# Optimization experiments

Measured on AMD Instinct MI355X. Metric: run time of the kernel, lower is better.

## Reference

```python
import jax, jax.numpy as jnp
import numpy as np

B = 16384
G = 2048   # granule_cell_count
N = 512    # ca3_cell_count
DT = 0.5   # integration_timestep
STEPS = 5  # ca3_attractor_steps
A_REC = 0.02   # recovery_time_constant
B_SUB = 0.2    # subthreshold_coupling
C_RESET = -55.0  # spike_reset_voltage
D_AHP = 4.0      # after_hyperpolarization_jump
CONN_P = 0.1


def setup_inputs() -> dict:
    key = jax.random.key(0)
    k1, k2, k3, k4 = jax.random.split(key, 4)
    dg_query_spikes = (jax.random.uniform(k1, (B, G)) < 0.1).astype(jnp.float32)
    W_mossy = 0.05 * jax.random.normal(k2, (N, G), dtype=jnp.float32)
    mask = (jax.random.uniform(k3, (N, N)) < CONN_P).astype(jnp.float32)
    W_rec = mask * jax.random.uniform(k4, (N, N)) * 0.1
    W_rec = W_rec * (1.0 - jnp.eye(N, dtype=jnp.float32))  # zero diagonal
    v0 = jnp.full((N,), -65.0, dtype=jnp.float32)
    u0 = jnp.full((N,), 0.2 * -65.0, dtype=jnp.float32)
    return {"dg_query_spikes": dg_query_spikes, "W_mossy": W_mossy,
            "W_rec": W_rec, "v0": v0, "u0": u0}


def _izhikevich_step(v, u, I):
    # Euler step of the Izhikevich neuron model, per original torch code.
    dv = 0.04 * v * v + 5.0 * v + 140.0 - u + I
    du = A_REC * (B_SUB * v - u)
    v = v + dv * DT
    u = u + du * DT
    spike = (v >= 30.0).astype(v.dtype)
    v = jnp.where(spike > 0, jnp.asarray(C_RESET, v.dtype), v)
    u = u + spike * D_AHP
    v = jnp.clip(v, -90.0, 30.0)
    return v, u, spike


def reference(dg_query_spikes, W_mossy, W_rec, v0, u0):
    # query_current = Linear(dg) * 10.0  -> [B, N]
    query_current = (dg_query_spikes @ W_mossy.T) * 10.0
    v = jnp.broadcast_to(v0, (B, N))
    u = jnp.broadcast_to(u0, (B, N))
    spike = jnp.zeros((B, N), dtype=jnp.float32)
    for _ in range(STEPS):  # fixed small unrolled recurrence
        # torch.mv(W_rec, spikes) batched: [B,N] @ [N,N]^T
        recurrent_current = (v >= 30.0).astype(jnp.float32) @ W_rec.T
        total_current = query_current + recurrent_current
        v, u, spike = _izhikevich_step(v, u, total_current)
    return spike
```

## Files before the change

### kernel.cpp

```cpp
#include <hip/hip_runtime.h>
#include <cstdint>
#include <cstddef>


typedef __attribute__((ext_vector_type(8))) short bf16x8;
typedef __attribute__((ext_vector_type(8))) unsigned short u16x8;
typedef __attribute__((ext_vector_type(4))) float f32x4;
typedef __attribute__((ext_vector_type(4))) unsigned int u32x4;

constexpr int Bn = 16384, Gn = 2048, Nn = 512;
constexpr int BM = 128, BN = 128, BK = 32;
constexpr int NKT = Gn / BK;
constexpr size_t A_BYTES = (size_t)NKT * 4 * Bn * 16;
constexpr size_t B_BYTES = (size_t)NKT * 3 * 4 * Nn * 16;

__device__ __forceinline__ unsigned short f2bf(float x) {
  uint32_t u = __builtin_bit_cast(uint32_t, x);
  u += 0x7FFFu + ((u >> 16) & 1u);
  return (unsigned short)(u >> 16);
}
__device__ __forceinline__ float bf2f(unsigned short h) {
  return __builtin_bit_cast(float, (uint32_t)h << 16);
}

__device__ __forceinline__ void glds16(const void* g, const void* l) {
  __builtin_amdgcn_global_load_lds(
      (const __attribute__((address_space(1))) unsigned int*)g,
      (__attribute__((address_space(3))) unsigned int*)l, 16, 0, 0);
}

__device__ __forceinline__ float izhi5(float I, float vi, float ui) {
#pragma clang fp contract(off)
  float v = vi, u = ui, spk = 0.0f;
#pragma unroll
  for (int st = 0; st < 5; ++st) {
    float dv = 0.04f * v * v + 5.0f * v + 140.0f - u + I;
    float du = 0.02f * (0.2f * v - u);
    v = v + dv * 0.5f;
    u = u + du * 0.5f;
    spk = (v >= 30.0f) ? 1.0f : 0.0f;
    if (spk > 0.0f) v = -55.0f;
    u = u + spk * 4.0f;
    v = fminf(fmaxf(v, -90.0f), 30.0f);
  }
  return spk;
}

__launch_bounds__(256)
__global__ void prep_dg(const float* __restrict__ dg, unsigned short* __restrict__ Ab) {
  __shared__ uint32_t lds[64][129];
  const int t  = (int)threadIdx.x;
  const int mt = (int)blockIdx.x >> 3;
  const int gt = (int)blockIdx.x & 7;
  const int m0 = mt * 64, g0 = gt * 256;
  {
    const int mm = t >> 2, q = t & 3;
    const float* src = dg + (size_t)(m0 + mm) * Gn + g0;
#pragma unroll
    for (int i = 0; i < 16; ++i) {
      float4 v = *reinterpret_cast<const float4*>(src + i * 16 + q * 4);
      uint32_t a = (v.x != 0.0f ? 0x3F80u : 0u) | (v.y != 0.0f ? 0x3F800000u : 0u);
      uint32_t b = (v.z != 0.0f ? 0x3F80u : 0u) | (v.w != 0.0f ? 0x3F800000u : 0u);
      const int c = i * 8 + q * 2;
      lds[mm][c] = a; lds[mm][c + 1] = b;
    }
  }
  __syncthreads();
  {
    const int mm = t & 63, c0 = t >> 6;
#pragma unroll
    for (int cc = 0; cc < 8; ++cc) {
      const int c = c0 + cc * 4;
      const int ktl = c >> 2, s = c & 3;
      const int cb = ktl * 16 + s * 4;
      u32x4 v;
      v.x = lds[mm][cb + 0]; v.y = lds[mm][cb + 1];
      v.z = lds[mm][cb + 2]; v.w = lds[mm][cb + 3];
      const size_t off = ((size_t)((gt * 8 + ktl) * 4 + s) * Bn + (m0 + mm)) * 16;
      *reinterpret_cast<u32x4*>(reinterpret_cast<char*>(Ab) + off) = v;
    }
  }
}

__launch_bounds__(256)
__global__ void prep_W(const float* __restrict__ Wm, unsigned short* __restrict__ Bb) {
  const int n  = (int)blockIdx.x;
  const int gi = (int)threadIdx.x;
  const float* src = Wm + (size_t)n * Gn + gi * 8;
  u16x8 h0, h1, h2;
#pragma unroll
  for (int e = 0; e < 8; ++e) {
    const float w  = src[e];
    const unsigned short b0 = f2bf(w);  const float f0 = bf2f(b0);
    const float r1 = w - f0;
    const unsigned short b1 = f2bf(r1); const float f1 = bf2f(b1);
    const float r2 = r1 - f1;
    const unsigned short b2 = f2bf(r2);
    h0[e] = b0; h1[e] = b1; h2[e] = b2;
  }
  const int kt = gi >> 2, s = gi & 3;
  char* base = reinterpret_cast<char*>(Bb);
  *reinterpret_cast<u16x8*>(base + ((size_t)((kt * 3 + 0) * 4 + s) * Nn + n) * 16) = h0;
  *reinterpret_cast<u16x8*>(base + ((size_t)((kt * 3 + 1) * 4 + s) * Nn + n) * 16) = h1;
  *reinterpret_cast<u16x8*>(base + ((size_t)((kt * 3 + 2) * 4 + s) * Nn + n) * 16) = h2;
}

__launch_bounds__(256, 2)
__global__ void gemm_spike(const char* __restrict__ Ab, const char* __restrict__ Bb,
                           const float* __restrict__ v0, const float* __restrict__ u0,
                           float* __restrict__ out) {
  __shared__ __align__(16) char lds[32768];
  const int t  = (int)threadIdx.x;
  const int bx = (int)blockIdx.x;
  const int mt = bx >> 2, nt = bx & 3;
  const int m0 = mt * BM, n0 = nt * BN;

  uint32_t asrc[2], bsrc[6];
#pragma unroll
  for (int c = 0; c < 2; ++c) {
    const int j = t + 256 * c;
    asrc[c] = (uint32_t)((((j >> 7) * Bn) + m0 + (j & 127)) * 16);
  }
#pragma unroll
  for (int c = 0; c < 6; ++c) {
    const int j = t + 256 * c;
    bsrc[c] = (uint32_t)(((((j >> 9) * 4 + ((j >> 7) & 3)) * Nn) + n0 + (j & 127)) * 16);
  }

  const int l  = t & 63, wv = t >> 6;
  const int wr = wv >> 1, wc = wv & 1;
  const int lr = l & 15, kh = l >> 4;

  uint32_t aoff[4], boff[3][4];
#pragma unroll
  for (int mf = 0; mf < 4; ++mf)
    aoff[mf] = (uint32_t)(((kh * 128) + wr * 64 + mf * 16 + lr) * 16);
#pragma unroll
  for (int p = 0; p < 3; ++p)
#pragma unroll
    for (int nf = 0; nf < 4; ++nf)
      boff[p][nf] = (uint32_t)(8192 + (((p * 4 + kh) * 128) + wc * 64 + nf * 16 + lr) * 16);

  f32x4 acc[4][4];
#pragma unroll
  for (int i = 0; i < 4; ++i)
#pragma unroll
    for (int j = 0; j < 4; ++j)
      acc[i][j] = (f32x4){0.0f, 0.0f, 0.0f, 0.0f};

  const char* pa = Ab;
  const char* pb = Bb;
  for (int kt = 0; kt < NKT; ++kt) {
    __syncthreads();
#pragma unroll
    for (int c = 0; c < 2; ++c) glds16(pa + asrc[c], &lds[(t + 256 * c) * 16]);
#pragma unroll
    for (int c = 0; c < 6; ++c) glds16(pb + bsrc[c], &lds[8192 + (t + 256 * c) * 16]);
    pa += (size_t)4 * Bn * 16;
    pb += (size_t)12 * Nn * 16;
    __syncthreads();

    bf16x8 af[4], bfr[3][4];
#pragma unroll
    for (int mf = 0; mf < 4; ++mf)
      af[mf] = *reinterpret_cast<const bf16x8*>(&lds[aoff[mf]]);
#pragma unroll
    for (int p = 0; p < 3; ++p)
#pragma unroll
      for (int nf = 0; nf < 4; ++nf)
        bfr[p][nf] = *reinterpret_cast<const bf16x8*>(&lds[boff[p][nf]]);
#pragma unroll
    for (int p = 0; p < 3; ++p)
#pragma unroll
      for (int mf = 0; mf < 4; ++mf)
#pragma unroll
        for (int nf = 0; nf < 4; ++nf)
          acc[mf][nf] = __builtin_amdgcn_mfma_f32_16x16x32_bf16(
              af[mf], bfr[p][nf], acc[mf][nf], 0, 0, 0);
  }

#pragma unroll
  for (int nf = 0; nf < 4; ++nf) {
    const int ncol = n0 + wc * 64 + nf * 16 + lr;
    const float vi = v0[ncol], ui = u0[ncol];
#pragma unroll
    for (int mf = 0; mf < 4; ++mf) {
      const int mrow = m0 + wr * 64 + mf * 16 + kh * 4;
#pragma unroll
      for (int r = 0; r < 4; ++r) {
        const float I = acc[mf][nf][r] * 10.0f;
        out[(size_t)(mrow + r) * Nn + ncol] = izhi5(I, vi, ui);
      }
    }
  }
}

constexpr int ROWS = 32, TG = 16, NCHUNK = Gn / 32;

__launch_bounds__(512, 2)
__global__ void ca3_sparse_kernel(const float* __restrict__ dg,
                                  const float* __restrict__ Wm,
                                  const float* __restrict__ v0,
                                  const float* __restrict__ u0,
                                  float* __restrict__ out) {
#pragma clang fp contract(off)
  __shared__ float    lds_w[TG * Nn];
  __shared__ uint32_t lds_bits[ROWS][NCHUNK];
  const int t    = (int)threadIdx.x;
  const int row0 = (int)blockIdx.x * ROWS;
  {
    const int r  = t >> 4;
    const int c0 = (t & 15) * 4;
    const float* p = dg + (size_t)(row0 + r) * Gn + (size_t)c0 * 32;
#pragma unroll
    for (int cc = 0; cc < 4; ++cc) {
      uint32_t bits = 0;
#pragma unroll
      for (int i = 0; i < 8; ++i) {
        float4 x = reinterpret_cast<const float4*>(p + cc * 32)[i];
        bits |= (x.x != 0.0f ? 1u : 0u) << (i * 4 + 0);
        bits |= (x.y != 0.0f ? 1u : 0u) << (i * 4 + 1);
        bits |= (x.z != 0.0f ? 1u : 0u) << (i * 4 + 2);
        bits |= (x.w != 0.0f ? 1u : 0u) << (i * 4 + 3);
      }
      lds_bits[r][c0 + cc] = bits;
    }
  }
  float acc[ROWS];
#pragma unroll
  for (int r = 0; r < ROWS; ++r) acc[r] = 0.0f;
  for (int gt = 0; gt < Gn / TG; ++gt) {
    __syncthreads();
    {
      const int k  = t & 3;
      const int nb = t >> 2;
#pragma unroll
      for (int pq = 0; pq < 4; ++pq) {
        const int n = pq * 128 + nb;
        const float4 w4 = *reinterpret_cast<const float4*>(
            Wm + (size_t)n * Gn + gt * TG + k * 4);
        lds_w[(k * 4 + 0) * Nn + n] = w4.x;
        lds_w[(k * 4 + 1) * Nn + n] = w4.y;
        lds_w[(k * 4 + 2) * Nn + n] = w4.z;
        lds_w[(k * 4 + 3) * Nn + n] = w4.w;
      }
    }
    __syncthreads();
    const int shift = (gt & 1) * 16;
#pragma unroll
    for (int r = 0; r < ROWS; ++r) {
      uint32_t b = (lds_bits[r][gt >> 1] >> shift) & 0xFFFFu;
      b = __builtin_amdgcn_readfirstlane(b);
      while (b) {
        const int g0 = __builtin_ctz(b);
        const uint32_t b1 = b & (b - 1);
        const int g1 = __builtin_ctz(b1 | 0x8000u);
        const uint32_t b2 = b1 & (b1 - 1);
        const int g2 = __builtin_ctz(b2 | 0x8000u);
        const uint32_t b3 = b2 & (b2 - 1);
        const int g3 = __builtin_ctz(b3 | 0x8000u);
        float x0 = lds_w[g0 * Nn + t];
        float x1 = lds_w[g1 * Nn + t];
        float x2 = lds_w[g2 * Nn + t];
        float x3 = lds_w[g3 * Nn + t];
        x1 = (b1 != 0u) ? x1 : 0.0f;
        x2 = (b2 != 0u) ? x2 : 0.0f;
        x3 = (b3 != 0u) ? x3 : 0.0f;
        acc[r] += x0; acc[r] += x1; acc[r] += x2; acc[r] += x3;
        b = b3 & (b3 - 1);
      }
    }
  }
  const float vi = v0[t];
  const float ui = u0[t];
#pragma unroll
  for (int r = 0; r < ROWS; ++r) {
    out[(size_t)(row0 + r) * Nn + t] = izhi5(acc[r] * 10.0f, vi, ui);
  }
}

extern "C" void kernel_launch(void* const* d_in, const int* in_sizes, int n_in,
                              void* d_out, int out_size, void* d_ws, size_t ws_size,
                              hipStream_t stream) {
  const float* dg = (const float*)d_in[0];
  const float* Wm = (const float*)d_in[1];
  const float* v0 = (const float*)d_in[3];
  const float* u0 = (const float*)d_in[4];
  float* out = (float*)d_out;

  if (ws_size < A_BYTES + B_BYTES) {
    hipLaunchKernelGGL(ca3_sparse_kernel, dim3(Bn / ROWS), dim3(512), 0, stream,
                       dg, Wm, v0, u0, out);
    return;
  }
  char* Ab = (char*)d_ws;
  char* Bb = (char*)d_ws + A_BYTES;
  hipLaunchKernelGGL(prep_dg, dim3(2048), dim3(256), 0, stream,
                     dg, (unsigned short*)Ab);
  hipLaunchKernelGGL(prep_W, dim3(512), dim3(256), 0, stream,
                     Wm, (unsigned short*)Bb);
  hipLaunchKernelGGL(gemm_spike, dim3(512), dim3(256), 0, stream,
                     Ab, Bb, v0, u0, out);
}
```

Baseline: 132.5 us.

## Double-buffer LDS tiles to overlap global loads with MFMA, remap block order

Replaces the single-buffered load/compute loop with a two-stage LDS ping-pong. The next K-slab is issued via global_load_lds before computing the current one, and there is a single barrier per iteration. It also remaps blockIdx so consecutive blocks spread across M tiles, which changes L2 locality and XCD distribution. LDS doubles to 64KB per block, which may limit occupancy at two blocks per CU.

```diff
diff --git a/kernel.cpp b/kernel.cpp
--- a/kernel.cpp
+++ b/kernel.cpp
@@ -11,8 +11,10 @@
 constexpr int Bn = 16384, Gn = 2048, Nn = 512;
 constexpr int BM = 128, BN = 128, BK = 32;
 constexpr int NKT = Gn / BK;
-constexpr size_t A_BYTES = (size_t)NKT * 4 * Bn * 16;
-constexpr size_t B_BYTES = (size_t)NKT * 3 * 4 * Nn * 16;
+constexpr size_t SLAB_A = (size_t)4 * Bn * 16;
+constexpr size_t SLAB_B = (size_t)12 * Nn * 16;
+constexpr size_t A_BYTES = (size_t)NKT * SLAB_A;
+constexpr size_t B_BYTES = (size_t)NKT * SLAB_B;
 
 __device__ __forceinline__ unsigned short f2bf(float x) {
   uint32_t u = __builtin_bit_cast(uint32_t, x);
@@ -109,9 +111,10 @@
 __global__ void gemm_spike(const char* __restrict__ Ab, const char* __restrict__ Bb,
                            const float* __restrict__ v0, const float* __restrict__ u0,
                            float* __restrict__ out) {
-  __shared__ __align__(16) char lds[32768];
-  const int t  = (int)threadIdx.x;
-  const int bx = (int)blockIdx.x;
+  __shared__ __align__(16) char lds[65536];
+  const int t = (int)threadIdx.x;
+  const int bx0 = (int)blockIdx.x;
+  const int bx  = (bx0 & 7) * 64 + (bx0 >> 3);
   const int mt = bx >> 2, nt = bx & 3;
   const int m0 = mt * BM, n0 = nt * BN;
 
@@ -148,27 +151,32 @@
     for (int j = 0; j < 4; ++j)
       acc[i][j] = (f32x4){0.0f, 0.0f, 0.0f, 0.0f};
 
-  const char* pa = Ab;
-  const char* pb = Bb;
+#pragma unroll
+  for (int c = 0; c < 2; ++c) glds16(Ab + asrc[c], &lds[(t + 256 * c) * 16]);
+#pragma unroll
+  for (int c = 0; c < 6; ++c) glds16(Bb + bsrc[c], &lds[8192 + (t + 256 * c) * 16]);
+  __syncthreads();
+
   for (int kt = 0; kt < NKT; ++kt) {
-    __syncthreads();
-#pragma unroll
-    for (int c = 0; c < 2; ++c) glds16(pa + asrc[c], &lds[(t + 256 * c) * 16]);
-#pragma unroll
-    for (int c = 0; c < 6; ++c) glds16(pb + bsrc[c], &lds[8192 + (t + 256 * c) * 16]);
-    pa += (size_t)4 * Bn * 16;
-    pb += (size_t)12 * Nn * 16;
-    __syncthreads();
-
+    const int cb = (kt & 1) << 15;
+    if (kt + 1 < NKT) {
+      const int nb = ((kt + 1) & 1) << 15;
+      const char* pa = Ab + (size_t)(kt + 1) * SLAB_A;
+      const char* pb = Bb + (size_t)(kt + 1) * SLAB_B;
+#pragma unroll
+      for (int c = 0; c < 2; ++c) glds16(pa + asrc[c], &lds[nb + (t + 256 * c) * 16]);
+#pragma unroll
+      for (int c = 0; c < 6; ++c) glds16(pb + bsrc[c], &lds[nb + 8192 + (t + 256 * c) * 16]);
+    }
     bf16x8 af[4], bfr[3][4];
 #pragma unroll
     for (int mf = 0; mf < 4; ++mf)
-      af[mf] = *reinterpret_cast<const bf16x8*>(&lds[aoff[mf]]);
+      af[mf] = *reinterpret_cast<const bf16x8*>(&lds[cb + aoff[mf]]);
 #pragma unroll
     for (int p = 0; p < 3; ++p)
 #pragma unroll
       for (int nf = 0; nf < 4; ++nf)
-        bfr[p][nf] = *reinterpret_cast<const bf16x8*>(&lds[boff[p][nf]]);
+        bfr[p][nf] = *reinterpret_cast<const bf16x8*>(&lds[cb + boff[p][nf]]);
 #pragma unroll
     for (int p = 0; p < 3; ++p)
 #pragma unroll
@@ -177,6 +185,7 @@
         for (int nf = 0; nf < 4; ++nf)
           acc[mf][nf] = __builtin_amdgcn_mfma_f32_16x16x32_bf16(
               af[mf], bfr[p][nf], acc[mf][nf], 0, 0, 0);
+    __syncthreads();
   }
 
 #pragma unroll
```

Result: faster. 121.7 us (-8.1%).
